# Performance work log

Hardware: AMD Instinct MI355X
Metric: run time of the kernel (lower is better)

The kernel has to match this reference:

```python
import jax, jax.numpy as jnp
import numpy as np

T, S, C = 256, 2048, 128
HID = 32      # MLP hidden (hardcoded in module)
G = 64        # gru_input_size
L = 64        # latent_size (GRU hidden)


def setup_inputs() -> dict:
    key = jax.random.key(0)
    ks = jax.random.split(key, 9)
    sc = lambda fan_in: 1.0 / np.sqrt(fan_in)
    return {
        "x": jax.random.normal(ks[0], (T, S, C), dtype=jnp.float32),
        # MLP: C -> 32 -> G, LeakyReLU after each layer
        "W1": jax.random.normal(ks[1], (C, HID), dtype=jnp.float32) * sc(C),
        "b1": jnp.zeros((HID,), jnp.float32),
        "W2": jax.random.normal(ks[2], (HID, G), dtype=jnp.float32) * sc(HID),
        "b2": jnp.zeros((G,), jnp.float32),
        # GRU params, PyTorch layout: W_ih (3L, G), W_hh (3L, L), gates ordered [r, z, n]
        "W_ih": jax.random.normal(ks[3], (3 * L, G), dtype=jnp.float32) * sc(L),
        "W_hh": jax.random.normal(ks[4], (3 * L, L), dtype=jnp.float32) * sc(L),
        "b_ih": jax.random.normal(ks[5], (3 * L,), dtype=jnp.float32) * sc(L),
        "b_hh": jax.random.normal(ks[6], (3 * L,), dtype=jnp.float32) * sc(L),
    }


def _lrelu(v):
    return jnp.where(v >= 0, v, 0.01 * v)


def reference(x, W1, b1, W2, b2, W_ih, W_hh, b_ih, b_hh):
    # Batched MLP projection over all (t, stock) pairs: (T,S,C) -> (T,S,G)
    h_proj = _lrelu(_lrelu(x @ W1 + b1) @ W2 + b2)

    # Precompute input-side gate activations for all timesteps: (T,S,3L)
    gx_all = h_proj @ W_ih.T + b_ih

    def step(h, gx):
        gh = h @ W_hh.T + b_hh  # (S, 3L)
        r = jax.nn.sigmoid(gx[:, :L] + gh[:, :L])
        z = jax.nn.sigmoid(gx[:, L:2 * L] + gh[:, L:2 * L])
        n = jnp.tanh(gx[:, 2 * L:] + r * gh[:, 2 * L:])
        h_new = (1.0 - z) * n + z * h
        return h_new, None

    h0 = jnp.zeros((S, L), jnp.float32)
    hT, _ = jax.lax.scan(step, h0, gx_all)
    return hT  # (stock_size, latent_size)
```

## Files before the change

### kernel.cpp

```cpp
#include <hip/hip_runtime.h>
#include <hip/hip_bf16.h>

#define T_TOT 256
#define S_TOT 2048
#define C_IN  128
#define HID_  32
#define G_    64
#define L_    64
#define TC    64
#define NCHUNK (T_TOT / TC)

typedef __attribute__((ext_vector_type(8))) short short8;
typedef __attribute__((ext_vector_type(4))) float f32x4;

#define MFMA(a, b, c) __builtin_amdgcn_mfma_f32_16x16x32_bf16((a), (b), (c), 0, 0, 0)

__device__ __forceinline__ void fsplit(float v, ushort& hi, ushort& lo) {
    __hip_bfloat16 h = __float2bfloat16(v);
    float hf = __bfloat162float(h);
    __hip_bfloat16 l = __float2bfloat16(v - hf);
    hi = *reinterpret_cast<ushort*>(&h);
    lo = *reinterpret_cast<ushort*>(&l);
}

__device__ __forceinline__ float lrelu(float v) { return v >= 0.f ? v : 0.01f * v; }

__device__ __forceinline__ float sig1(float x) {
    x = fminf(fmaxf(x, -30.f), 30.f);
    return __builtin_amdgcn_rcpf(1.f + __expf(-x));
}
__device__ __forceinline__ float th1(float x) {
    x = fminf(fmaxf(x, -15.f), 15.f);
    float e = __expf(-2.f * x);
    return (1.f - e) * __builtin_amdgcn_rcpf(1.f + e);
}

__global__ __launch_bounds__(256, 2)
void mlp_kernel(const float* __restrict__ x,
                const float* __restrict__ W1, const float* __restrict__ b1,
                const float* __restrict__ W2, const float* __restrict__ b2,
                float* __restrict__ hpws)
{
    __shared__ ushort w1h[32][128], w1l[32][128];
    __shared__ ushort w2h[64][32],  w2l[64][32];
    __shared__ ushort xh[4][16][128], xl[4][16][128];
    __shared__ ushort h1h[4][16][32], h1l[4][16][32];

    const int tid = threadIdx.x;
    const int w = tid >> 6, l = tid & 63;
    const int lg = l >> 4, lr = l & 15;

#pragma unroll
    for (int i = 0; i < 16; ++i) {
        int e = tid + 256 * i;
        int k = e >> 5, n = e & 31;
        ushort hi, lo; fsplit(W1[e], hi, lo);
        int by = (2 * k) ^ ((n & 7) << 4);
        *(ushort*)((char*)&w1h[n][0] + by) = hi;
        *(ushort*)((char*)&w1l[n][0] + by) = lo;
    }
#pragma unroll
    for (int i = 0; i < 8; ++i) {
        int e = tid + 256 * i;
        int k = e >> 6, n = e & 63;
        ushort hi, lo; fsplit(W2[e], hi, lo);
        int by = (2 * k) ^ ((n & 3) << 4);
        *(ushort*)((char*)&w2h[n][0] + by) = hi;
        *(ushort*)((char*)&w2l[n][0] + by) = lo;
    }

    const size_t row0 = (size_t)blockIdx.x * 64 + w * 16;
    const float4* xg = (const float4*)(x + row0 * C_IN);
#pragma unroll
    for (int i = 0; i < 8; ++i) {
        int f4 = l + 64 * i;
        int r = f4 >> 5, c4 = f4 & 31;
        float4 v = xg[f4];
        ushort h4[4], l4[4];
        fsplit(v.x, h4[0], l4[0]);
        fsplit(v.y, h4[1], l4[1]);
        fsplit(v.z, h4[2], l4[2]);
        fsplit(v.w, h4[3], l4[3]);
        int by = (8 * c4) ^ ((r & 7) << 4);
        ushort4 ph = {h4[0], h4[1], h4[2], h4[3]};
        ushort4 pl = {l4[0], l4[1], l4[2], l4[3]};
        *(ushort4*)((char*)&xh[w][r][0] + by) = ph;
        *(ushort4*)((char*)&xl[w][r][0] + by) = pl;
    }
    __syncthreads();

    f32x4 h1acc[2];
#pragma unroll
    for (int nt = 0; nt < 2; ++nt) {
        int col = lr + 16 * nt;
        float bb = b1[col];
        f32x4 acc = {bb, bb, bb, bb};
#pragma unroll
        for (int ks = 0; ks < 4; ++ks) {
            int aby = (64 * ks + 16 * lg) ^ ((lr & 7) << 4);
            short8 ahi = *(short8*)((char*)&xh[w][lr][0] + aby);
            short8 alo = *(short8*)((char*)&xl[w][lr][0] + aby);
            int bby = (64 * ks + 16 * lg) ^ ((col & 7) << 4);
            short8 bhi = *(short8*)((char*)&w1h[col][0] + bby);
            short8 blo = *(short8*)((char*)&w1l[col][0] + bby);
            acc = MFMA(ahi, bhi, acc);
            acc = MFMA(ahi, blo, acc);
            acc = MFMA(alo, bhi, acc);
        }
        h1acc[nt] = acc;
    }
#pragma unroll
    for (int nt = 0; nt < 2; ++nt) {
        int col = lr + 16 * nt;
#pragma unroll
        for (int r = 0; r < 4; ++r) {
            float v = lrelu(h1acc[nt][r]);
            ushort hi, lo; fsplit(v, hi, lo);
            int row = 4 * lg + r;
            int by = (2 * col) ^ ((row & 3) << 4);
            *(ushort*)((char*)&h1h[w][row][0] + by) = hi;
            *(ushort*)((char*)&h1l[w][row][0] + by) = lo;
        }
    }
    __syncthreads();

    f32x4 hpacc[4];
#pragma unroll
    for (int nt = 0; nt < 4; ++nt) {
        int col = lr + 16 * nt;
        float bb = b2[col];
        f32x4 acc = {bb, bb, bb, bb};
        int aby = (16 * lg) ^ ((lr & 3) << 4);
        short8 ahi = *(short8*)((char*)&h1h[w][lr][0] + aby);
        short8 alo = *(short8*)((char*)&h1l[w][lr][0] + aby);
        int bby = (16 * lg) ^ ((col & 3) << 4);
        short8 bhi = *(short8*)((char*)&w2h[col][0] + bby);
        short8 blo = *(short8*)((char*)&w2l[col][0] + bby);
        acc = MFMA(ahi, bhi, acc);
        acc = MFMA(ahi, blo, acc);
        acc = MFMA(alo, bhi, acc);
        hpacc[nt] = acc;
    }
    __syncthreads();
#pragma unroll
    for (int nt = 0; nt < 4; ++nt) {
        int col = lr + 16 * nt;
#pragma unroll
        for (int r = 0; r < 4; ++r) {
            float v = lrelu(hpacc[nt][r]);
            ushort hi, lo; fsplit(v, hi, lo);
            int row = 4 * lg + r;
            int by = (2 * col) ^ ((row & 7) << 4);
            *(ushort*)((char*)&xh[w][row][0] + by) = hi;
            *(ushort*)((char*)&xl[w][row][0] + by) = lo;
        }
    }
    __syncthreads();

    const size_t rt = row0 >> 4;
    float4* outw = (float4*)hpws;
#pragma unroll
    for (int ks = 0; ks < 2; ++ks) {
        int by = (64 * ks + 16 * lg) ^ ((lr & 7) << 4);
        short8 fh = *(short8*)((char*)&xh[w][lr][0] + by);
        short8 fl = *(short8*)((char*)&xl[w][lr][0] + by);
        outw[((rt * 2 + ks) * 2 + 0) * 64 + l] = *(float4*)&fh;
        outw[((rt * 2 + ks) * 2 + 1) * 64 + l] = *(float4*)&fl;
    }
}

__global__ __launch_bounds__(256, 1)
void gru_kernel(const float* __restrict__ hpws_f,
                const float* __restrict__ W_ih, const float* __restrict__ W_hh,
                const float* __restrict__ b_ih, const float* __restrict__ b_hh,
                float* __restrict__ out, int first)
{
    __shared__ ushort hh_[16][64], hl_[16][64];

    const int tid = threadIdx.x;
    const int w = tid >> 6, l = tid & 63;
    const int lg = l >> 4, lr = l & 15;
    const int colr = 16 * w + lr;
    const int b = blockIdx.x;

    short8 wih_h[3][2], wih_l[3][2], whh_h[3][2], whh_l[3][2];
    float bih[3], bhh[3];
#pragma unroll
    for (int g = 0; g < 3; ++g) {
        int n = colr + 64 * g;
        bih[g] = b_ih[n];
        bhh[g] = b_hh[n];
#pragma unroll
        for (int ks = 0; ks < 2; ++ks) {
            const float* p = W_ih + n * 64 + 32 * ks + 8 * lg;
            const float* q = W_hh + n * 64 + 32 * ks + 8 * lg;
            short8 ph, pl, qh, ql;
#pragma unroll
            for (int j = 0; j < 8; ++j) {
                ushort hi, lo;
                fsplit(p[j], hi, lo); ph[j] = (short)hi; pl[j] = (short)lo;
                fsplit(q[j], hi, lo); qh[j] = (short)hi; ql[j] = (short)lo;
            }
            wih_h[g][ks] = ph; wih_l[g][ks] = pl;
            whh_h[g][ks] = qh; whh_l[g][ks] = ql;
        }
    }

    f32x4 hprev;
#pragma unroll
    for (int r = 0; r < 4; ++r) {
        int s = 16 * b + 4 * lg + r;
        hprev[r] = first ? 0.f : out[s * 64 + colr];
    }
#pragma unroll
    for (int r = 0; r < 4; ++r) {
        ushort hi, lo; fsplit(hprev[r], hi, lo);
        int row = 4 * lg + r;
        int by = (2 * colr) ^ ((row & 7) << 4);
        *(ushort*)((char*)&hh_[row][0] + by) = hi;
        *(ushort*)((char*)&hl_[row][0] + by) = lo;
    }
    __syncthreads();

    const short8* hpg = (const short8*)hpws_f;
    short8 cur[2][2], nxt[2][2];
    {
        size_t rt = (size_t)b;
#pragma unroll
        for (int ks = 0; ks < 2; ++ks)
#pragma unroll
            for (int pl = 0; pl < 2; ++pl)
                cur[ks][pl] = hpg[((rt * 2 + ks) * 2 + pl) * 64 + l];
    }

    for (int t = 0; t < TC; ++t) {
        if (t + 1 < TC) {
            size_t rt = (size_t)(t + 1) * 128 + b;
#pragma unroll
            for (int ks = 0; ks < 2; ++ks)
#pragma unroll
                for (int pl = 0; pl < 2; ++pl)
                    nxt[ks][pl] = hpg[((rt * 2 + ks) * 2 + pl) * 64 + l];
        }

        f32x4 agx[3], agh[3];
#pragma unroll
        for (int g = 0; g < 3; ++g) {
            float bb = bih[g];
            agx[g] = {bb, bb, bb, bb};
        }
#pragma unroll
        for (int ks = 0; ks < 2; ++ks)
#pragma unroll
            for (int g = 0; g < 3; ++g) {
                agx[g] = MFMA(cur[ks][0], wih_h[g][ks], agx[g]);
                agx[g] = MFMA(cur[ks][0], wih_l[g][ks], agx[g]);
                agx[g] = MFMA(cur[ks][1], wih_h[g][ks], agx[g]);
            }

        short8 ah[2], al[2];
#pragma unroll
        for (int ks = 0; ks < 2; ++ks) {
            int by = (64 * ks + 16 * lg) ^ ((lr & 7) << 4);
            ah[ks] = *(short8*)((char*)&hh_[lr][0] + by);
            al[ks] = *(short8*)((char*)&hl_[lr][0] + by);
        }
#pragma unroll
        for (int g = 0; g < 3; ++g) {
            float bb = bhh[g];
            agh[g] = {bb, bb, bb, bb};
        }
#pragma unroll
        for (int ks = 0; ks < 2; ++ks)
#pragma unroll
            for (int g = 0; g < 3; ++g) {
                agh[g] = MFMA(ah[ks], whh_h[g][ks], agh[g]);
                agh[g] = MFMA(ah[ks], whh_l[g][ks], agh[g]);
                agh[g] = MFMA(al[ks], whh_h[g][ks], agh[g]);
            }

        f32x4 hn;
#pragma unroll
        for (int r = 0; r < 4; ++r) {
            float rr = sig1(agx[0][r] + agh[0][r]);
            float zz = sig1(agx[1][r] + agh[1][r]);
            float nn = th1(agx[2][r] + rr * agh[2][r]);
            hn[r] = (1.f - zz) * nn + zz * hprev[r];
        }

        __syncthreads();
#pragma unroll
        for (int r = 0; r < 4; ++r) {
            ushort hi, lo; fsplit(hn[r], hi, lo);
            int row = 4 * lg + r;
            int by = (2 * colr) ^ ((row & 7) << 4);
            *(ushort*)((char*)&hh_[row][0] + by) = hi;
            *(ushort*)((char*)&hl_[row][0] + by) = lo;
        }
        hprev = hn;
        __syncthreads();

#pragma unroll
        for (int ks = 0; ks < 2; ++ks)
#pragma unroll
            for (int pl = 0; pl < 2; ++pl)
                cur[ks][pl] = nxt[ks][pl];
    }

#pragma unroll
    for (int r = 0; r < 4; ++r)
        out[(16 * b + 4 * lg + r) * 64 + colr] = hprev[r];
}

extern "C" void kernel_launch(void* const* d_in, const int* in_sizes, int n_in,
                              void* d_out, int out_size, void* d_ws, size_t ws_size,
                              hipStream_t stream)
{
    const float* x    = (const float*)d_in[0];
    const float* W1   = (const float*)d_in[1];
    const float* b1   = (const float*)d_in[2];
    const float* W2   = (const float*)d_in[3];
    const float* b2   = (const float*)d_in[4];
    const float* W_ih = (const float*)d_in[5];
    const float* W_hh = (const float*)d_in[6];
    const float* b_ih = (const float*)d_in[7];
    const float* b_hh = (const float*)d_in[8];
    float* out  = (float*)d_out;
    float* hpws = (float*)d_ws;

    for (int c = 0; c < NCHUNK; ++c) {
        mlp_kernel<<<(TC * S_TOT) / 64, 256, 0, stream>>>(
            x + (size_t)c * TC * S_TOT * C_IN, W1, b1, W2, b2, hpws);
        gru_kernel<<<S_TOT / 16, 256, 0, stream>>>(
            hpws, W_ih, W_hh, b_ih, b_hh, out, c == 0 ? 1 : 0);
    }
}
```

Before: 609.9 us.

## Run whole sequence in one GRU launch with double-buffered hidden state

Replaces the four-chunk MLP+GRU launch loop with one MLP launch over all timesteps and one GRU launch over all 256 steps, so the hidden state no longer round-trips through global memory between chunks. The hidden state in LDS is double-buffered, which cuts the per-step barriers from two to one, and projected inputs are prefetched two steps ahead through a three-slot register ring. The MFMA accumulation is split into three independent chains per gate to shorten dependency latency. The workspace must now hold projections for all timesteps, and the one remaining barrier is raw inline asm.

```diff
diff --git a/kernel.cpp b/kernel.cpp
--- a/kernel.cpp
+++ b/kernel.cpp
@@ -7,8 +7,6 @@
 #define HID_  32
 #define G_    64
 #define L_    64
-#define TC    64
-#define NCHUNK (T_TOT / TC)
 
 typedef __attribute__((ext_vector_type(8))) short short8;
 typedef __attribute__((ext_vector_type(4))) float f32x4;
@@ -169,19 +167,101 @@
     }
 }
 
+__device__ __forceinline__ void gstep(
+    const short8 (&cur)[2][2], short8 (&pf)[2][2], int t,
+    const short8* __restrict__ hpg, int b, int l, int lg, int lr, int colr,
+    const short8 (&wih_h)[3][2], const short8 (&wih_l)[3][2],
+    const short8 (&whh_h)[3][2], const short8 (&whh_l)[3][2],
+    const float (&bih)[3], const float (&bhh)[3],
+    f32x4& hprev, int& p, ushort* hbh, ushort* hbl)
+{
+    if (t + 2 < T_TOT) {
+        size_t rt = (size_t)(t + 2) * 128 + b;
+#pragma unroll
+        for (int ks = 0; ks < 2; ++ks)
+#pragma unroll
+            for (int pl = 0; pl < 2; ++pl)
+                pf[ks][pl] = hpg[((rt * 2 + ks) * 2 + pl) * 64 + l];
+    }
+
+    const ushort* rh = hbh + p * 1024;
+    const ushort* rl = hbl + p * 1024;
+    short8 ah[2], al[2];
+#pragma unroll
+    for (int ks = 0; ks < 2; ++ks) {
+        int by = (64 * ks + 16 * lg) ^ ((lr & 7) << 4);
+        ah[ks] = *(short8*)((char*)(rh + lr * 64) + by);
+        al[ks] = *(short8*)((char*)(rl + lr * 64) + by);
+    }
+
+    f32x4 agx[3], agh[3];
+#pragma unroll
+    for (int g = 0; g < 3; ++g) {
+        f32x4 c0 = {bih[g], bih[g], bih[g], bih[g]};
+        f32x4 c1 = {0.f, 0.f, 0.f, 0.f};
+        f32x4 c2 = {0.f, 0.f, 0.f, 0.f};
+        c0 = MFMA(cur[0][0], wih_h[g][0], c0);
+        c1 = MFMA(cur[0][0], wih_l[g][0], c1);
+        c2 = MFMA(cur[0][1], wih_h[g][0], c2);
+        c0 = MFMA(cur[1][0], wih_h[g][1], c0);
+        c1 = MFMA(cur[1][0], wih_l[g][1], c1);
+        c2 = MFMA(cur[1][1], wih_h[g][1], c2);
+        agx[g] = c0 + c1 + c2;
+    }
+#pragma unroll
+    for (int g = 0; g < 3; ++g) {
+        f32x4 c0 = {bhh[g], bhh[g], bhh[g], bhh[g]};
+        f32x4 c1 = {0.f, 0.f, 0.f, 0.f};
+        f32x4 c2 = {0.f, 0.f, 0.f, 0.f};
+        c0 = MFMA(ah[0], whh_h[g][0], c0);
+        c1 = MFMA(ah[0], whh_l[g][0], c1);
+        c2 = MFMA(al[0], whh_h[g][0], c2);
+        c0 = MFMA(ah[1], whh_h[g][1], c0);
+        c1 = MFMA(ah[1], whh_l[g][1], c1);
+        c2 = MFMA(al[1], whh_h[g][1], c2);
+        agh[g] = c0 + c1 + c2;
+    }
+
+    f32x4 hn;
+#pragma unroll
+    for (int r = 0; r < 4; ++r) {
+        float rr = sig1(agx[0][r] + agh[0][r]);
+        float zz = sig1(agx[1][r] + agh[1][r]);
+        float nn = th1(agx[2][r] + rr * agh[2][r]);
+        hn[r] = (1.f - zz) * nn + zz * hprev[r];
+    }
+
+    ushort* wh = hbh + (p ^ 1) * 1024;
+    ushort* wl = hbl + (p ^ 1) * 1024;
+#pragma unroll
+    for (int r = 0; r < 4; ++r) {
+        ushort hi, lo; fsplit(hn[r], hi, lo);
+        int row = 4 * lg + r;
+        int by = (2 * colr) ^ ((row & 7) << 4);
+        *(ushort*)((char*)(wh + row * 64) + by) = hi;
+        *(ushort*)((char*)(wl + row * 64) + by) = lo;
+    }
+    hprev = hn;
+
+    asm volatile("s_waitcnt lgkmcnt(0)\n\ts_barrier" ::: "memory");
+    p ^= 1;
+}
+
 __global__ __launch_bounds__(256, 1)
 void gru_kernel(const float* __restrict__ hpws_f,
                 const float* __restrict__ W_ih, const float* __restrict__ W_hh,
                 const float* __restrict__ b_ih, const float* __restrict__ b_hh,
-                float* __restrict__ out, int first)
+                float* __restrict__ out)
 {
-    __shared__ ushort hh_[16][64], hl_[16][64];
+    __shared__ ushort hbh_s[2][16][64], hbl_s[2][16][64];
 
     const int tid = threadIdx.x;
     const int w = tid >> 6, l = tid & 63;
     const int lg = l >> 4, lr = l & 15;
     const int colr = 16 * w + lr;
     const int b = blockIdx.x;
+    ushort* hbh = &hbh_s[0][0][0];
+    ushort* hbl = &hbl_s[0][0][0];
 
     short8 wih_h[3][2], wih_l[3][2], whh_h[3][2], whh_l[3][2];
     float bih[3], bhh[3];
@@ -192,120 +272,53 @@
         bhh[g] = b_hh[n];
 #pragma unroll
         for (int ks = 0; ks < 2; ++ks) {
-            const float* p = W_ih + n * 64 + 32 * ks + 8 * lg;
-            const float* q = W_hh + n * 64 + 32 * ks + 8 * lg;
+            const float* pp = W_ih + n * 64 + 32 * ks + 8 * lg;
+            const float* qq = W_hh + n * 64 + 32 * ks + 8 * lg;
             short8 ph, pl, qh, ql;
 #pragma unroll
             for (int j = 0; j < 8; ++j) {
                 ushort hi, lo;
-                fsplit(p[j], hi, lo); ph[j] = (short)hi; pl[j] = (short)lo;
-                fsplit(q[j], hi, lo); qh[j] = (short)hi; ql[j] = (short)lo;
+                fsplit(pp[j], hi, lo); ph[j] = (short)hi; pl[j] = (short)lo;
+                fsplit(qq[j], hi, lo); qh[j] = (short)hi; ql[j] = (short)lo;
             }
             wih_h[g][ks] = ph; wih_l[g][ks] = pl;
             whh_h[g][ks] = qh; whh_l[g][ks] = ql;
         }
     }
 
-    f32x4 hprev;
+    f32x4 hprev = {0.f, 0.f, 0.f, 0.f};
 #pragma unroll
     for (int r = 0; r < 4; ++r) {
-        int s = 16 * b + 4 * lg + r;
-        hprev[r] = first ? 0.f : out[s * 64 + colr];
-    }
-#pragma unroll
-    for (int r = 0; r < 4; ++r) {
-        ushort hi, lo; fsplit(hprev[r], hi, lo);
         int row = 4 * lg + r;
         int by = (2 * colr) ^ ((row & 7) << 4);
-        *(ushort*)((char*)&hh_[row][0] + by) = hi;
-        *(ushort*)((char*)&hl_[row][0] + by) = lo;
-    }
-    __syncthreads();
+        *(ushort*)((char*)(hbh + row * 64) + by) = 0;
+        *(ushort*)((char*)(hbl + row * 64) + by) = 0;
+    }
+    asm volatile("s_waitcnt lgkmcnt(0)\n\ts_barrier" ::: "memory");
+    int p = 0;
 
     const short8* hpg = (const short8*)hpws_f;
-    short8 cur[2][2], nxt[2][2];
-    {
-        size_t rt = (size_t)b;
+    short8 ring[3][2][2];
+#pragma unroll
+    for (int tt = 0; tt < 2; ++tt) {
+        size_t rt = (size_t)tt * 128 + b;
 #pragma unroll
         for (int ks = 0; ks < 2; ++ks)
 #pragma unroll
             for (int pl = 0; pl < 2; ++pl)
-                cur[ks][pl] = hpg[((rt * 2 + ks) * 2 + pl) * 64 + l];
-    }
-
-    for (int t = 0; t < TC; ++t) {
-        if (t + 1 < TC) {
-            size_t rt = (size_t)(t + 1) * 128 + b;
-#pragma unroll
-            for (int ks = 0; ks < 2; ++ks)
-#pragma unroll
-                for (int pl = 0; pl < 2; ++pl)
-                    nxt[ks][pl] = hpg[((rt * 2 + ks) * 2 + pl) * 64 + l];
-        }
-
-        f32x4 agx[3], agh[3];
-#pragma unroll
-        for (int g = 0; g < 3; ++g) {
-            float bb = bih[g];
-            agx[g] = {bb, bb, bb, bb};
-        }
-#pragma unroll
-        for (int ks = 0; ks < 2; ++ks)
-#pragma unroll
-            for (int g = 0; g < 3; ++g) {
-                agx[g] = MFMA(cur[ks][0], wih_h[g][ks], agx[g]);
-                agx[g] = MFMA(cur[ks][0], wih_l[g][ks], agx[g]);
-                agx[g] = MFMA(cur[ks][1], wih_h[g][ks], agx[g]);
-            }
-
-        short8 ah[2], al[2];
-#pragma unroll
-        for (int ks = 0; ks < 2; ++ks) {
-            int by = (64 * ks + 16 * lg) ^ ((lr & 7) << 4);
-            ah[ks] = *(short8*)((char*)&hh_[lr][0] + by);
-            al[ks] = *(short8*)((char*)&hl_[lr][0] + by);
-        }
-#pragma unroll
-        for (int g = 0; g < 3; ++g) {
-            float bb = bhh[g];
-            agh[g] = {bb, bb, bb, bb};
-        }
-#pragma unroll
-        for (int ks = 0; ks < 2; ++ks)
-#pragma unroll
-            for (int g = 0; g < 3; ++g) {
-                agh[g] = MFMA(ah[ks], whh_h[g][ks], agh[g]);
-                agh[g] = MFMA(ah[ks], whh_l[g][ks], agh[g]);
-                agh[g] = MFMA(al[ks], whh_h[g][ks], agh[g]);
-            }
-
-        f32x4 hn;
-#pragma unroll
-        for (int r = 0; r < 4; ++r) {
-            float rr = sig1(agx[0][r] + agh[0][r]);
-            float zz = sig1(agx[1][r] + agh[1][r]);
-            float nn = th1(agx[2][r] + rr * agh[2][r]);
-            hn[r] = (1.f - zz) * nn + zz * hprev[r];
-        }
-
-        __syncthreads();
-#pragma unroll
-        for (int r = 0; r < 4; ++r) {
-            ushort hi, lo; fsplit(hn[r], hi, lo);
-            int row = 4 * lg + r;
-            int by = (2 * colr) ^ ((row & 7) << 4);
-            *(ushort*)((char*)&hh_[row][0] + by) = hi;
-            *(ushort*)((char*)&hl_[row][0] + by) = lo;
-        }
-        hprev = hn;
-        __syncthreads();
-
-#pragma unroll
-        for (int ks = 0; ks < 2; ++ks)
-#pragma unroll
-            for (int pl = 0; pl < 2; ++pl)
-                cur[ks][pl] = nxt[ks][pl];
-    }
+                ring[tt][ks][pl] = hpg[((rt * 2 + ks) * 2 + pl) * 64 + l];
+    }
+
+    for (int tb = 0; tb < 255; tb += 3) {
+        gstep(ring[0], ring[2], tb + 0, hpg, b, l, lg, lr, colr,
+              wih_h, wih_l, whh_h, whh_l, bih, bhh, hprev, p, hbh, hbl);
+        gstep(ring[1], ring[0], tb + 1, hpg, b, l, lg, lr, colr,
+              wih_h, wih_l, whh_h, whh_l, bih, bhh, hprev, p, hbh, hbl);
+        gstep(ring[2], ring[1], tb + 2, hpg, b, l, lg, lr, colr,
+              wih_h, wih_l, whh_h, whh_l, bih, bhh, hprev, p, hbh, hbl);
+    }
+    gstep(ring[0], ring[2], 255, hpg, b, l, lg, lr, colr,
+          wih_h, wih_l, whh_h, whh_l, bih, bhh, hprev, p, hbh, hbl);
 
 #pragma unroll
     for (int r = 0; r < 4; ++r)
@@ -328,10 +341,6 @@
     float* out  = (float*)d_out;
     float* hpws = (float*)d_ws;
 
-    for (int c = 0; c < NCHUNK; ++c) {
-        mlp_kernel<<<(TC * S_TOT) / 64, 256, 0, stream>>>(
-            x + (size_t)c * TC * S_TOT * C_IN, W1, b1, W2, b2, hpws);
-        gru_kernel<<<S_TOT / 16, 256, 0, stream>>>(
-            hpws, W_ih, W_hh, b_ih, b_hh, out, c == 0 ? 1 : 0);
-    }
-}
+    mlp_kernel<<<(T_TOT * S_TOT) / 64, 256, 0, stream>>>(x, W1, b1, W2, b2, hpws);
+    gru_kernel<<<S_TOT / 16, 256, 0, stream>>>(hpws, W_ih, W_hh, b_ih, b_hh, out);
+}
```

New measurement: 606.1 us. No clear change (-0.6%).
